# Performance work log

Measured on AMD Instinct MI355X. Metric: run time of the kernel, lower is better.

The kernel has to match this reference:

```python
import jax, jax.numpy as jnp
import numpy as np

VOCAB = 32000
DIM = 1024
BATCH = 2
SEQ = 2048
CHUNK = 256
LCTX = 4            # local_context_size, mode='sum'
LOCAL_WIN = 512     # sparse_local_window (>= 2*chunk)
GSTRIDE = 1024      # sparse_global_stride (>= 4*chunk)
LN_EPS = 1e-5


def _cache_positions():
    """Simulate the deterministic sparse KV-cache pruning per chunk (numpy, trace-time).
    Returns list of key-position index arrays (cached positions ++ current chunk)."""
    cache = np.zeros((0,), dtype=np.int64)
    per_chunk = []
    for i in range(SEQ // CHUNK):
        new = np.arange(i * CHUNK, (i + 1) * CHUNK, dtype=np.int64)
        full = np.concatenate([cache, new])
        per_chunk.append(full)
        total_seen = (i + 1) * CHUNK
        local_start = max(0, total_seen - LOCAL_WIN)
        keep = (full >= local_start) | (full % GSTRIDE == 0)
        cache = full[keep]
    return per_chunk


def setup_inputs() -> dict:
    key = jax.random.key(0)
    ks = jax.random.split(key, 8)
    s = 0.02
    return {
        "x": jax.random.randint(ks[0], (BATCH, SEQ), 0, VOCAB, dtype=jnp.int64),
        "emb_table": jax.random.normal(ks[1], (VOCAB, DIM), jnp.float32) * s,
        "q_w": jax.random.normal(ks[2], (DIM, DIM), jnp.float32) * s,
        "q_b": jnp.zeros((DIM,), jnp.float32),
        "k_w": jax.random.normal(ks[3], (DIM, DIM), jnp.float32) * s,
        "k_b": jnp.zeros((DIM,), jnp.float32),
        "v_w": jax.random.normal(ks[4], (DIM, DIM), jnp.float32) * s,
        "v_b": jnp.zeros((DIM,), jnp.float32),
        "o_w": jax.random.normal(ks[5], (DIM, DIM), jnp.float32) * s,
        "o_b": jnp.zeros((DIM,), jnp.float32),
        "ln_w": jnp.ones((DIM,), jnp.float32),
        "ln_b": jnp.zeros((DIM,), jnp.float32),
        "out_w": jax.random.normal(ks[6], (VOCAB, DIM), jnp.float32) * s,
        "out_b": jnp.zeros((VOCAB,), jnp.float32),
    }


def reference(x, emb_table, q_w, q_b, k_w, k_b, v_w, v_b, o_w, o_b, ln_w, ln_b, out_w, out_b):
    # embedding + causal local context (sum of 0..LCTX-1 shifted embeddings)
    emb = emb_table[x]                                  # [B,S,D]
    ctx = emb
    for off in range(1, LCTX):
        ctx = ctx + jnp.pad(emb, ((0, 0), (off, 0), (0, 0)))[:, :SEQ]

    # project full sequence once (same per-chunk projections in the original)
    Q = ctx @ q_w.T + q_b                               # [B,S,D]
    K = ctx @ k_w.T + k_b
    V = ctx @ v_w.T + v_b
    scale = 1.0 / np.sqrt(DIM).astype(np.float32)

    outs = []
    for i, kpos in enumerate(_cache_positions()):
        qpos = np.arange(i * CHUNK, (i + 1) * CHUNK, dtype=np.int64)
        q = Q[:, i * CHUNK:(i + 1) * CHUNK]             # [B,C,D]
        k = K[:, kpos]                                  # [B,Ki,D] gathered sparse cache + chunk
        v = V[:, kpos]
        scores = jnp.einsum('bqd,bkd->bqk', q, k) * scale
        mask = kpos[None, :] > qpos[:, None]            # [C,Ki] static causal mask
        scores = jnp.where(mask[None, :, :], -jnp.inf, scores)
        w = jax.nn.softmax(scores, axis=-1)
        outs.append(jnp.einsum('bqk,bkd->bqd', w, v))

    attended = jnp.concatenate(outs, axis=1)            # [B,S,D]
    h = attended @ o_w.T + o_b
    # LayerNorm
    mu = h.mean(-1, keepdims=True)
    var = ((h - mu) ** 2).mean(-1, keepdims=True)
    h = (h - mu) / jnp.sqrt(var + LN_EPS) * ln_w + ln_b
    return h @ out_w.T + out_b                          # [B,S,VOCAB]
```

## Files before the change

### kernel.cpp

```cpp
#include <hip/hip_runtime.h>
#include <stdint.h>

#define DIMN 1024
#define SEQN 2048
#define BATCHN 2
#define NCHUNK 8
#define CHUNKSZ 256
#define VOCABN 32000
#define ROWS_PB 6016
#define PSTRIDE_B (256*ROWS_PB)
#define LN_EPS 1e-5f

#define MBIG 4096
#define NBIG 32000
#define KBIG 1024
#define NTILES_K (KBIG/64)

typedef unsigned short ushort_t;
typedef __attribute__((ext_vector_type(8))) __bf16 bf16x8;
typedef __attribute__((ext_vector_type(4))) float f32x4;

__device__ const int d_nk[8]   = {256,512,768,769,769,769,769,770};
__device__ const int d_np[8]   = {256,512,768,896,896,896,896,896};
__device__ const int d_koff[8] = {0,256,768,1536,2432,3328,4224,5120};

__device__ __forceinline__ ushort_t f2bu(float f) {
  union { float f; unsigned u; } v; v.f = f;
  unsigned r = v.u + 0x7FFFu + ((v.u >> 16) & 1u);
  return (ushort_t)(r >> 16);
}
__device__ __forceinline__ float b2f(ushort_t u) {
  union { unsigned u; float f; } v; v.u = ((unsigned)u) << 16; return v.f;
}

__device__ __forceinline__ int pos_of(int i, int j) {
  if (i <= 2) return j;
  if (i <= 6) return (j == 0) ? 0 : (i - 3) * 256 + 255 + j;
  return (j == 0) ? 0 : ((j == 1) ? 1024 : 1278 + j);
}

__device__ __forceinline__ void gload16(const void* g, void* l) {
  __builtin_amdgcn_global_load_lds((__attribute__((address_space(1))) void*)g,
                                   (__attribute__((address_space(3))) void*)l,
                                   16, 0, 0);
}

__device__ __forceinline__ void mma_core_s(const ushort_t* __restrict__ A,
                                           const ushort_t* __restrict__ Bt,
                                           int K, ushort_t* lA, ushort_t* lB,
                                           f32x4 acc[4][4], int tid) {
  const int lane = tid & 63;
  const int wr = (tid >> 7) & 1;
  const int wc = (tid >> 6) & 1;
  const int frow = lane & 15;
  const int lhi = lane >> 4;
  const int xk = (frow & 7) << 4;
  const size_t ldb = (size_t)K * 2;
  for (int kt = 0; kt < K; kt += 64) {
#pragma unroll
    for (int t = 0; t < 4; ++t) {
      int cid = t * 256 + tid;
      int row = cid >> 3;
      int srcoff = ((cid & 7) * 16) ^ ((row & 7) << 4);
      gload16((const char*)A  + (size_t)row * ldb + (size_t)kt * 2 + srcoff,
              (char*)lA + cid * 16);
      gload16((const char*)Bt + (size_t)row * ldb + (size_t)kt * 2 + srcoff,
              (char*)lB + cid * 16);
    }
    __syncthreads();
#pragma unroll
    for (int kk = 0; kk < 2; ++kk) {
      bf16x8 af[4], bfr[4];
#pragma unroll
      for (int m = 0; m < 4; ++m) {
        int r = wr * 64 + m * 16 + frow;
        af[m] = *(const bf16x8*)((const char*)lA +
                 ((r * 128 + kk * 64 + lhi * 16) ^ xk));
      }
#pragma unroll
      for (int n = 0; n < 4; ++n) {
        int r = wc * 64 + n * 16 + frow;
        bfr[n] = *(const bf16x8*)((const char*)lB +
                  ((r * 128 + kk * 64 + lhi * 16) ^ xk));
      }
#pragma unroll
      for (int m = 0; m < 4; ++m)
#pragma unroll
        for (int n = 0; n < 4; ++n)
          acc[m][n] = __builtin_amdgcn_mfma_f32_16x16x32_bf16(af[m], bfr[n],
                                                              acc[m][n], 0, 0, 0);
    }
    __syncthreads();
  }
}

__device__ __forceinline__ void stage_tile_big(const char* Abase, const char* Bbase,
                                               ushort_t* ldsbuf, int ktile, int tid) {
  const size_t ldb = (size_t)KBIG * 2;
#pragma unroll
  for (int s = 0; s < 4; ++s) {
    const char* base = (s < 2 ? Abase : Bbase) + (size_t)(s & 1) * 128 * ldb
                       + (size_t)ktile * 128;
    ushort_t* lh = ldsbuf + s * 8192;
#pragma unroll
    for (int r2 = 0; r2 < 2; ++r2) {
      int c = r2 * 512 + tid;
      int row = c >> 3;
      int off_l = (c * 16) ^ ((row & 7) << 4);
      gload16(base + (size_t)row * ldb + (off_l & 127), (char*)lh + c * 16);
    }
  }
}

__global__ __launch_bounds__(512, 2) void k_vocab(
    const ushort_t* __restrict__ A, const ushort_t* __restrict__ Bt,
    const float* __restrict__ bias, float* __restrict__ C) {
  __shared__ ushort_t lds[2][4][8192];
  const int tid = threadIdx.x;
  const int lane = tid & 63, w = tid >> 6, wm = w >> 2, wn = w & 3;
  const int frow = lane & 15, lhi = lane >> 4;
  const int xk = (frow & 7) << 4;

  int l = blockIdx.x;
  int swz = (l & 7) * ((int)gridDim.x >> 3) + (l >> 3);
  const int mt = swz & 15;
  const int nt = swz >> 4;
  const char* Abase = (const char*)(A + (size_t)mt * 256 * KBIG);
  const char* Bbase = (const char*)(Bt + (size_t)nt * 256 * KBIG);

  f32x4 acc[8][4] = {};

  stage_tile_big(Abase, Bbase, &lds[0][0][0], 0, tid);

  for (int kt = 0; kt < NTILES_K; ++kt) {
    const int cur = kt & 1;
    __builtin_amdgcn_sched_barrier(0);
    if (kt + 1 < NTILES_K) {
      stage_tile_big(Abase, Bbase, &lds[cur ^ 1][0][0], kt + 1, tid);
      asm volatile("s_waitcnt vmcnt(8)");
    } else {
      asm volatile("s_waitcnt vmcnt(0)");
    }
    __builtin_amdgcn_s_barrier();
    __builtin_amdgcn_sched_barrier(0);

    const char* lA = (const char*)&lds[cur][wm][0];
    const char* lB = (const char*)&lds[cur][2 + (wn >> 1)][0];

    bf16x8 bF[4][2];
#pragma unroll
    for (int fc = 0; fc < 4; ++fc) {
      int c = (wn & 1) * 64 + fc * 16 + frow;
#pragma unroll
      for (int kk = 0; kk < 2; ++kk)
        bF[fc][kk] = *(const bf16x8*)(lB + ((c * 128 + kk * 64 + lhi * 16) ^ xk));
    }
#pragma unroll
    for (int q = 0; q < 4; ++q) {
      bf16x8 aF[2][2];
#pragma unroll
      for (int i = 0; i < 2; ++i) {
        int r = (2 * q + i) * 16 + frow;
#pragma unroll
        for (int kk = 0; kk < 2; ++kk)
          aF[i][kk] = *(const bf16x8*)(lA + ((r * 128 + kk * 64 + lhi * 16) ^ xk));
      }
      if (q) __builtin_amdgcn_s_barrier();
      __builtin_amdgcn_s_setprio(1);
#pragma unroll
      for (int i = 0; i < 2; ++i)
#pragma unroll
        for (int fc = 0; fc < 4; ++fc)
#pragma unroll
          for (int kk = 0; kk < 2; ++kk)
            acc[2 * q + i][fc] = __builtin_amdgcn_mfma_f32_16x16x32_bf16(
                aF[i][kk], bF[fc][kk], acc[2 * q + i][fc], 0, 0, 0);
      __builtin_amdgcn_s_setprio(0);
    }
    __builtin_amdgcn_s_barrier();
  }

  const int rbase = mt * 256 + wm * 128 + lhi * 4;
  const int cbase = nt * 256 + wn * 64 + frow;
#pragma unroll
  for (int fc = 0; fc < 4; ++fc) {
    float bv = bias[cbase + fc * 16];
#pragma unroll
    for (int fr = 0; fr < 8; ++fr)
#pragma unroll
      for (int j = 0; j < 4; ++j)
        C[(size_t)(rbase + fr * 16 + j) * NBIG + cbase + fc * 16] =
            acc[fr][fc][j] + bv;
  }
}

__global__ __launch_bounds__(256) void k_cvt(const float* __restrict__ src,
                                             ushort_t* __restrict__ dst, int n) {
  int idx = blockIdx.x * 256 + threadIdx.x;
  int stride = gridDim.x * 256;
  int n4 = n >> 2;
  for (int i = idx; i < n4; i += stride) {
    float4 v = ((const float4*)src)[i];
    ((ushort4*)dst)[i] = make_ushort4(f2bu(v.x), f2bu(v.y), f2bu(v.z), f2bu(v.w));
  }
}

__global__ __launch_bounds__(256) void k_embed(const int* __restrict__ x,
                                               const float* __restrict__ emb,
                                               ushort_t* __restrict__ ctxb) {
  const int t = blockIdx.x, b = blockIdx.y, tid = threadIdx.x;
  float4 s = make_float4(0.f, 0.f, 0.f, 0.f);
#pragma unroll
  for (int o = 0; o < 4; ++o) {
    if (t - o < 0) break;
    int tok = x[b * SEQN + t - o];
    float4 v = ((const float4*)(emb + (size_t)tok * DIMN))[tid];
    s.x += v.x; s.y += v.y; s.z += v.z; s.w += v.w;
  }
  ((ushort4*)(ctxb + ((size_t)(b * SEQN + t)) * DIMN))[tid] =
      make_ushort4(f2bu(s.x), f2bu(s.y), f2bu(s.z), f2bu(s.w));
}

__global__ __launch_bounds__(256) void k_qkv(const ushort_t* __restrict__ A,
    const ushort_t* __restrict__ Bt, const float* __restrict__ qb2,
    const float* __restrict__ kb2, const float* __restrict__ vb2,
    ushort_t* __restrict__ Qb, ushort_t* __restrict__ Kb,
    ushort_t* __restrict__ Vb) {
  __shared__ __align__(16) ushort_t lA[128*64];
  __shared__ __align__(16) ushort_t lB[128*64];
  f32x4 acc[4][4] = {};
  const int tid = threadIdx.x;
  mma_core_s(A + (size_t)blockIdx.y * 128 * KBIG,
             Bt + (size_t)blockIdx.x * 128 * KBIG, KBIG, lA, lB, acc, tid);
  const int which = blockIdx.x >> 3;
  const int col0  = (blockIdx.x & 7) * 128;
  ushort_t* Out = (which == 0) ? Qb : (which == 1) ? Kb : Vb;
  const float* Bv = (which == 0) ? qb2 : (which == 1) ? kb2 : vb2;
  const int lane = tid & 63, wr = (tid >> 7) & 1, wc = (tid >> 6) & 1;
  const int rbase = blockIdx.y * 128 + wr * 64 + (lane >> 4) * 4;
  const int cbase = col0 + wc * 64 + (lane & 15);
#pragma unroll
  for (int m = 0; m < 4; ++m)
#pragma unroll
    for (int n = 0; n < 4; ++n) {
      int c = cbase + n * 16;
      float bv = Bv[c];
#pragma unroll
      for (int j = 0; j < 4; ++j)
        Out[(size_t)(rbase + m * 16 + j) * DIMN + c] = f2bu(acc[m][n][j] + bv);
    }
}

__global__ __launch_bounds__(256) void k_gemm_f32(const ushort_t* __restrict__ A,
    const ushort_t* __restrict__ Bt, const float* __restrict__ bias,
    float* __restrict__ C, int N, int K) {
  __shared__ __align__(16) ushort_t lA[128*64];
  __shared__ __align__(16) ushort_t lB[128*64];
  f32x4 acc[4][4] = {};
  const int tid = threadIdx.x;
  mma_core_s(A + (size_t)blockIdx.y * 128 * K, Bt + (size_t)blockIdx.x * 128 * K,
             K, lA, lB, acc, tid);
  const int lane = tid & 63, wr = (tid >> 7) & 1, wc = (tid >> 6) & 1;
  const int rbase = blockIdx.y * 128 + wr * 64 + (lane >> 4) * 4;
  const int cbase = blockIdx.x * 128 + wc * 64 + (lane & 15);
#pragma unroll
  for (int m = 0; m < 4; ++m)
#pragma unroll
    for (int n = 0; n < 4; ++n) {
      int c = cbase + n * 16;
      float bv = bias[c];
#pragma unroll
      for (int j = 0; j < 4; ++j)
        C[(size_t)(rbase + m * 16 + j) * N + c] = acc[m][n][j] + bv;
    }
}

__global__ __launch_bounds__(256) void k_gatherK(const ushort_t* __restrict__ Kb,
                                                 ushort_t* __restrict__ Kg) {
  const int r = blockIdx.x, b = blockIdx.y, tid = threadIdx.x;
  int i = 7;
#pragma unroll
  for (int q = 0; q < 7; ++q) if (r < d_koff[q + 1]) { i = q; break; }
  const int j = r - d_koff[i];
  ushort4* dst = (ushort4*)(Kg + ((size_t)b * ROWS_PB + r) * DIMN);
  if (j < d_nk[i]) {
    int pos = pos_of(i, j);
    dst[tid] = ((const ushort4*)(Kb + ((size_t)b * SEQN + pos) * DIMN))[tid];
  } else {
    dst[tid] = make_ushort4(0, 0, 0, 0);
  }
}

__global__ __launch_bounds__(256) void k_transV(const ushort_t* __restrict__ Vb,
                                                ushort_t* __restrict__ VgT) {
  __shared__ ushort_t tile[64][66];
  const int z = blockIdx.z, b = z >> 3, i = z & 7;
  const int np = d_np[i], nk = d_nk[i], ko = d_koff[i];
  const int jb = blockIdx.x * 64;
  if (jb >= np) return;
  const int db = blockIdx.y * 64;
  const int tid = threadIdx.x, tx = tid & 63, ty = tid >> 6;
#pragma unroll
  for (int rep = 0; rep < 16; ++rep) {
    int jl = rep * 4 + ty;
    int j = jb + jl;
    ushort_t v = 0;
    if (j < nk) v = Vb[((size_t)b * SEQN + pos_of(i, j)) * DIMN + db + tx];
    tile[jl][tx] = v;
  }
  __syncthreads();
  const size_t base = ((size_t)b * ROWS_PB + ko) * DIMN;
#pragma unroll
  for (int rep = 0; rep < 16; ++rep) {
    int dl = rep * 4 + ty;
    VgT[base + (size_t)(db + dl) * np + jb + tx] = tile[tx][dl];
  }
}

__global__ __launch_bounds__(256) void k_scores(const ushort_t* __restrict__ Qb,
    const ushort_t* __restrict__ Kg, ushort_t* __restrict__ P) {
  const int z = blockIdx.z, b = z >> 3, i = z & 7;
  const int np = d_np[i], nk = d_nk[i], ko = d_koff[i];
  if ((int)blockIdx.x * 128 >= np) return;
  __shared__ __align__(16) ushort_t lA[128*64];
  __shared__ __align__(16) ushort_t lB[128*64];
  f32x4 acc[4][4] = {};
  const int tid = threadIdx.x;
  const ushort_t* A  = Qb + ((size_t)(b * SEQN + i * CHUNKSZ) + blockIdx.y * 128) * DIMN;
  const ushort_t* Bt = Kg + ((size_t)b * ROWS_PB + ko + blockIdx.x * 128) * DIMN;
  mma_core_s(A, Bt, DIMN, lA, lB, acc, tid);
  const int lane = tid & 63, wr = (tid >> 7) & 1, wc = (tid >> 6) & 1;
  const int rb = blockIdx.y * 128 + wr * 64 + (lane >> 4) * 4;
  const int cb = blockIdx.x * 128 + wc * 64 + (lane & 15);
  ushort_t* Pc = P + (size_t)b * PSTRIDE_B + (size_t)ko * 256;
  const float scale = 0.03125f;
  const int diag0 = nk - CHUNKSZ;
#pragma unroll
  for (int m = 0; m < 4; ++m)
#pragma unroll
    for (int n = 0; n < 4; ++n) {
      int c = cb + n * 16;
#pragma unroll
      for (int j = 0; j < 4; ++j) {
        int r = rb + m * 16 + j;
        float w = 0.0f;
        if (c < nk && (c - diag0) <= r) w = expf(acc[m][n][j] * scale);
        Pc[(size_t)r * np + c] = f2bu(w);
      }
    }
}

__global__ __launch_bounds__(256) void k_rowsum(const ushort_t* __restrict__ P,
                                                float* __restrict__ rowsum) {
  const int z = blockIdx.y, b = z >> 3, i = z & 7, r = blockIdx.x;
  const int np = d_np[i], ko = d_koff[i];
  const ushort_t* row = P + (size_t)b * PSTRIDE_B + (size_t)ko * 256 + (size_t)r * np;
  const int tid = threadIdx.x;
  float s = 0.f;
  for (int c = tid; c < np; c += 256) s += b2f(row[c]);
#pragma unroll
  for (int o = 1; o < 64; o <<= 1) s += __shfl_xor(s, o);
  __shared__ float ss[4];
  if ((tid & 63) == 0) ss[tid >> 6] = s;
  __syncthreads();
  if (tid == 0) rowsum[z * 256 + r] = ss[0] + ss[1] + ss[2] + ss[3];
}

__global__ __launch_bounds__(256) void k_pv(const ushort_t* __restrict__ P,
    const ushort_t* __restrict__ VgT, const float* __restrict__ rowsum,
    ushort_t* __restrict__ attb) {
  const int z = blockIdx.z, b = z >> 3, i = z & 7;
  const int np = d_np[i], ko = d_koff[i];
  __shared__ __align__(16) ushort_t lA[128*64];
  __shared__ __align__(16) ushort_t lB[128*64];
  f32x4 acc[4][4] = {};
  const int tid = threadIdx.x;
  const ushort_t* A  = P + (size_t)b * PSTRIDE_B + (size_t)ko * 256 +
                       (size_t)blockIdx.y * 128 * np;
  const ushort_t* Bt = VgT + ((size_t)b * ROWS_PB + ko) * DIMN +
                       (size_t)blockIdx.x * 128 * np;
  mma_core_s(A, Bt, np, lA, lB, acc, tid);
  const int lane = tid & 63, wr = (tid >> 7) & 1, wc = (tid >> 6) & 1;
  const int rb = blockIdx.y * 128 + wr * 64 + (lane >> 4) * 4;
  const int cb = blockIdx.x * 128 + wc * 64 + (lane & 15);
  const float* rs = rowsum + z * 256;
  ushort_t* outp = attb + (size_t)(b * SEQN + i * CHUNKSZ) * DIMN;
#pragma unroll
  for (int m = 0; m < 4; ++m)
#pragma unroll
    for (int j = 0; j < 4; ++j) {
      int r = rb + m * 16 + j;
      float inv = 1.0f / rs[r];
#pragma unroll
      for (int n = 0; n < 4; ++n)
        outp[(size_t)r * DIMN + cb + n * 16] = f2bu(acc[m][n][j] * inv);
    }
}

__global__ __launch_bounds__(256) void k_ln(const float* __restrict__ h,
    const float* __restrict__ lnw, const float* __restrict__ lnb,
    ushort_t* __restrict__ hb) {
  const int row = blockIdx.x, tid = threadIdx.x;
  float4 v = ((const float4*)(h + (size_t)row * DIMN))[tid];
  float s  = v.x + v.y + v.z + v.w;
  float sq = v.x * v.x + v.y * v.y + v.z * v.z + v.w * v.w;
#pragma unroll
  for (int o = 1; o < 64; o <<= 1) { s += __shfl_xor(s, o); sq += __shfl_xor(sq, o); }
  __shared__ float ss[4], ssq[4];
  if ((tid & 63) == 0) { ss[tid >> 6] = s; ssq[tid >> 6] = sq; }
  __syncthreads();
  s  = ss[0] + ss[1] + ss[2] + ss[3];
  sq = ssq[0] + ssq[1] + ssq[2] + ssq[3];
  const float mu  = s * (1.0f / DIMN);
  const float var = sq * (1.0f / DIMN) - mu * mu;
  const float inv = rsqrtf(var + LN_EPS);
  float4 w4 = ((const float4*)lnw)[tid];
  float4 b4 = ((const float4*)lnb)[tid];
  ushort4 o4 = make_ushort4(f2bu((v.x - mu) * inv * w4.x + b4.x),
                            f2bu((v.y - mu) * inv * w4.y + b4.y),
                            f2bu((v.z - mu) * inv * w4.z + b4.z),
                            f2bu((v.w - mu) * inv * w4.w + b4.w));
  ((ushort4*)(hb + (size_t)row * DIMN))[tid] = o4;
}

extern "C" void kernel_launch(void* const* d_in, const int* in_sizes, int n_in,
                              void* d_out, int out_size, void* d_ws, size_t ws_size,
                              hipStream_t stream) {
  const int*   x    = (const int*)  d_in[0];
  const float* emb  = (const float*)d_in[1];
  const float* qw   = (const float*)d_in[2];
  const float* qb   = (const float*)d_in[3];
  const float* kw   = (const float*)d_in[4];
  const float* kb   = (const float*)d_in[5];
  const float* vw   = (const float*)d_in[6];
  const float* vb   = (const float*)d_in[7];
  const float* ow   = (const float*)d_in[8];
  const float* ob   = (const float*)d_in[9];
  const float* lnw  = (const float*)d_in[10];
  const float* lnb  = (const float*)d_in[11];
  const float* outw = (const float*)d_in[12];
  const float* outb = (const float*)d_in[13];
  float* out = (float*)d_out;
  (void)in_sizes; (void)n_in; (void)out_size; (void)ws_size;

  char* ws = (char*)d_ws;
  size_t off = 0;
  auto alloc = [&](size_t bytes) {
    size_t r = off; off += (bytes + 255) & ~(size_t)255; return r;
  };
  ushort_t* wqkvb = (ushort_t*)(ws + alloc((size_t)3 * DIMN * DIMN * 2));
  ushort_t* wob   = (ushort_t*)(ws + alloc((size_t)DIMN * DIMN * 2));
  ushort_t* woutb = (ushort_t*)(ws + alloc((size_t)VOCABN * DIMN * 2));
  ushort_t* ctxb  = (ushort_t*)(ws + alloc((size_t)BATCHN * SEQN * DIMN * 2));
  ushort_t* Qb    = (ushort_t*)(ws + alloc((size_t)BATCHN * SEQN * DIMN * 2));
  ushort_t* Kb    = (ushort_t*)(ws + alloc((size_t)BATCHN * SEQN * DIMN * 2));
  ushort_t* Vb    = (ushort_t*)(ws + alloc((size_t)BATCHN * SEQN * DIMN * 2));
  ushort_t* Kg    = (ushort_t*)(ws + alloc((size_t)BATCHN * ROWS_PB * DIMN * 2));
  ushort_t* VgT   = (ushort_t*)(ws + alloc((size_t)BATCHN * ROWS_PB * DIMN * 2));
  ushort_t* Pm    = (ushort_t*)(ws + alloc((size_t)BATCHN * PSTRIDE_B * 2));
  float*    rsum  = (float*)   (ws + alloc((size_t)BATCHN * NCHUNK * 256 * 4));
  ushort_t* attb  = (ushort_t*)(ws + alloc((size_t)BATCHN * SEQN * DIMN * 2));
  float*    hbuf  = (float*)   (ws + alloc((size_t)BATCHN * SEQN * DIMN * 4));
  ushort_t* hb    = (ushort_t*)(ws + alloc((size_t)BATCHN * SEQN * DIMN * 2));

  k_cvt<<<dim3(1024), dim3(256), 0, stream>>>(qw, wqkvb,                 DIMN * DIMN);
  k_cvt<<<dim3(1024), dim3(256), 0, stream>>>(kw, wqkvb + DIMN * DIMN,   DIMN * DIMN);
  k_cvt<<<dim3(1024), dim3(256), 0, stream>>>(vw, wqkvb + 2 * DIMN * DIMN, DIMN * DIMN);
  k_cvt<<<dim3(1024), dim3(256), 0, stream>>>(ow,   wob,   DIMN * DIMN);
  k_cvt<<<dim3(2048), dim3(256), 0, stream>>>(outw, woutb, VOCABN * DIMN);

  k_embed<<<dim3(SEQN, BATCHN), dim3(256), 0, stream>>>(x, emb, ctxb);

  k_qkv<<<dim3(24, 32), dim3(256), 0, stream>>>(ctxb, wqkvb, qb, kb, vb,
                                                Qb, Kb, Vb);

  k_gatherK<<<dim3(ROWS_PB, BATCHN), dim3(256), 0, stream>>>(Kb, Kg);
  k_transV<<<dim3(14, 16, BATCHN * NCHUNK), dim3(256), 0, stream>>>(Vb, VgT);

  k_scores<<<dim3(7, 2, BATCHN * NCHUNK), dim3(256), 0, stream>>>(Qb, Kg, Pm);
  k_rowsum<<<dim3(256, BATCHN * NCHUNK), dim3(256), 0, stream>>>(Pm, rsum);
  k_pv<<<dim3(8, 2, BATCHN * NCHUNK), dim3(256), 0, stream>>>(Pm, VgT, rsum, attb);

  k_gemm_f32<<<dim3(8, 32), dim3(256), 0, stream>>>(attb, wob, ob, hbuf, DIMN, DIMN);
  k_ln<<<dim3(BATCHN * SEQN), dim3(256), 0, stream>>>(hbuf, lnw, lnb, hb);

  k_vocab<<<dim3(2000), dim3(512), 0, stream>>>(hb, woutb, outb, out);
}
```

Baseline: 604.4 us.

## Merge weight conversions, swizzle QKV grid, store o-proj output as bf16

Replaces five weight-conversion launches with one merged kernel to cut launch overhead. Remaps the QKV GEMM to a 1D grid with an XCD-style swizzle so tiles that share data land on the same chiplet and reuse cache. Writes the output projection in bf16 instead of fp32, which halves the traffic into LayerNorm at the cost of rounding h to bf16 before normalization.

```diff
diff --git a/kernel.cpp b/kernel.cpp
--- a/kernel.cpp
+++ b/kernel.cpp
@@ -194,14 +194,30 @@
   }
 }
 
-__global__ __launch_bounds__(256) void k_cvt(const float* __restrict__ src,
-                                             ushort_t* __restrict__ dst, int n) {
+#define SEG (DIMN*DIMN/4)
+__global__ __launch_bounds__(256) void k_cvt5(
+    const float* __restrict__ qw, const float* __restrict__ kw,
+    const float* __restrict__ vw, const float* __restrict__ ow,
+    const float* __restrict__ outw, ushort_t* __restrict__ wqkvb,
+    ushort_t* __restrict__ wob, ushort_t* __restrict__ woutb) {
+  const int total = 4 * SEG + (VOCABN * DIMN / 4);
   int idx = blockIdx.x * 256 + threadIdx.x;
   int stride = gridDim.x * 256;
-  int n4 = n >> 2;
-  for (int i = idx; i < n4; i += stride) {
-    float4 v = ((const float4*)src)[i];
-    ((ushort4*)dst)[i] = make_ushort4(f2bu(v.x), f2bu(v.y), f2bu(v.z), f2bu(v.w));
+  for (int i = idx; i < total; i += stride) {
+    const float4* src; ushort4* dst;
+    if (i < 3 * SEG) {
+      src = (const float4*)(i < SEG ? qw : i < 2 * SEG ? kw : vw) +
+            (i - (i < SEG ? 0 : i < 2 * SEG ? SEG : 2 * SEG));
+      dst = (ushort4*)wqkvb + i;
+    } else if (i < 4 * SEG) {
+      src = (const float4*)ow + (i - 3 * SEG);
+      dst = (ushort4*)wob + (i - 3 * SEG);
+    } else {
+      src = (const float4*)outw + (i - 4 * SEG);
+      dst = (ushort4*)woutb + (i - 4 * SEG);
+    }
+    float4 v = *src;
+    *dst = make_ushort4(f2bu(v.x), f2bu(v.y), f2bu(v.z), f2bu(v.w));
   }
 }
 
@@ -226,40 +242,44 @@
     const float* __restrict__ kb2, const float* __restrict__ vb2,
     ushort_t* __restrict__ Qb, ushort_t* __restrict__ Kb,
     ushort_t* __restrict__ Vb) {
+  int l = blockIdx.x;
+  int swz = (l & 7) * ((int)gridDim.x >> 3) + (l >> 3);
+  const int mt = swz & 31;
+  const int nt = swz >> 5;
+  __shared__ __align__(16) ushort_t lA[128*64];
+  __shared__ __align__(16) ushort_t lB[128*64];
+  f32x4 acc[4][4] = {};
+  const int tid = threadIdx.x;
+  mma_core_s(A + (size_t)mt * 128 * KBIG,
+             Bt + (size_t)nt * 128 * KBIG, KBIG, lA, lB, acc, tid);
+  const int which = nt >> 3;
+  const int col0  = (nt & 7) * 128;
+  ushort_t* Out = (which == 0) ? Qb : (which == 1) ? Kb : Vb;
+  const float* Bv = (which == 0) ? qb2 : (which == 1) ? kb2 : vb2;
+  const int lane = tid & 63, wr = (tid >> 7) & 1, wc = (tid >> 6) & 1;
+  const int rbase = mt * 128 + wr * 64 + (lane >> 4) * 4;
+  const int cbase = col0 + wc * 64 + (lane & 15);
+#pragma unroll
+  for (int m = 0; m < 4; ++m)
+#pragma unroll
+    for (int n = 0; n < 4; ++n) {
+      int c = cbase + n * 16;
+      float bv = Bv[c];
+#pragma unroll
+      for (int j = 0; j < 4; ++j)
+        Out[(size_t)(rbase + m * 16 + j) * DIMN + c] = f2bu(acc[m][n][j] + bv);
+    }
+}
+
+__global__ __launch_bounds__(256) void k_oproj(const ushort_t* __restrict__ A,
+    const ushort_t* __restrict__ Bt, const float* __restrict__ bias,
+    ushort_t* __restrict__ C) {
   __shared__ __align__(16) ushort_t lA[128*64];
   __shared__ __align__(16) ushort_t lB[128*64];
   f32x4 acc[4][4] = {};
   const int tid = threadIdx.x;
   mma_core_s(A + (size_t)blockIdx.y * 128 * KBIG,
              Bt + (size_t)blockIdx.x * 128 * KBIG, KBIG, lA, lB, acc, tid);
-  const int which = blockIdx.x >> 3;
-  const int col0  = (blockIdx.x & 7) * 128;
-  ushort_t* Out = (which == 0) ? Qb : (which == 1) ? Kb : Vb;
-  const float* Bv = (which == 0) ? qb2 : (which == 1) ? kb2 : vb2;
-  const int lane = tid & 63, wr = (tid >> 7) & 1, wc = (tid >> 6) & 1;
-  const int rbase = blockIdx.y * 128 + wr * 64 + (lane >> 4) * 4;
-  const int cbase = col0 + wc * 64 + (lane & 15);
-#pragma unroll
-  for (int m = 0; m < 4; ++m)
-#pragma unroll
-    for (int n = 0; n < 4; ++n) {
-      int c = cbase + n * 16;
-      float bv = Bv[c];
-#pragma unroll
-      for (int j = 0; j < 4; ++j)
-        Out[(size_t)(rbase + m * 16 + j) * DIMN + c] = f2bu(acc[m][n][j] + bv);
-    }
-}
-
-__global__ __launch_bounds__(256) void k_gemm_f32(const ushort_t* __restrict__ A,
-    const ushort_t* __restrict__ Bt, const float* __restrict__ bias,
-    float* __restrict__ C, int N, int K) {
-  __shared__ __align__(16) ushort_t lA[128*64];
-  __shared__ __align__(16) ushort_t lB[128*64];
-  f32x4 acc[4][4] = {};
-  const int tid = threadIdx.x;
-  mma_core_s(A + (size_t)blockIdx.y * 128 * K, Bt + (size_t)blockIdx.x * 128 * K,
-             K, lA, lB, acc, tid);
   const int lane = tid & 63, wr = (tid >> 7) & 1, wc = (tid >> 6) & 1;
   const int rbase = blockIdx.y * 128 + wr * 64 + (lane >> 4) * 4;
   const int cbase = blockIdx.x * 128 + wc * 64 + (lane & 15);
@@ -271,7 +291,7 @@
       float bv = bias[c];
 #pragma unroll
       for (int j = 0; j < 4; ++j)
-        C[(size_t)(rbase + m * 16 + j) * N + c] = acc[m][n][j] + bv;
+        C[(size_t)(rbase + m * 16 + j) * DIMN + c] = f2bu(acc[m][n][j] + bv);
     }
 }
 
@@ -397,11 +417,12 @@
     }
 }
 
-__global__ __launch_bounds__(256) void k_ln(const float* __restrict__ h,
+__global__ __launch_bounds__(256) void k_ln(const ushort_t* __restrict__ h,
     const float* __restrict__ lnw, const float* __restrict__ lnb,
     ushort_t* __restrict__ hb) {
   const int row = blockIdx.x, tid = threadIdx.x;
-  float4 v = ((const float4*)(h + (size_t)row * DIMN))[tid];
+  ushort4 u4 = ((const ushort4*)(h + (size_t)row * DIMN))[tid];
+  float4 v = make_float4(b2f(u4.x), b2f(u4.y), b2f(u4.z), b2f(u4.w));
   float s  = v.x + v.y + v.z + v.w;
   float sq = v.x * v.x + v.y * v.y + v.z * v.z + v.w * v.w;
 #pragma unroll
@@ -460,19 +481,16 @@
   ushort_t* Pm    = (ushort_t*)(ws + alloc((size_t)BATCHN * PSTRIDE_B * 2));
   float*    rsum  = (float*)   (ws + alloc((size_t)BATCHN * NCHUNK * 256 * 4));
   ushort_t* attb  = (ushort_t*)(ws + alloc((size_t)BATCHN * SEQN * DIMN * 2));
-  float*    hbuf  = (float*)   (ws + alloc((size_t)BATCHN * SEQN * DIMN * 4));
+  ushort_t* hbuf  = (ushort_t*)(ws + alloc((size_t)BATCHN * SEQN * DIMN * 2));
   ushort_t* hb    = (ushort_t*)(ws + alloc((size_t)BATCHN * SEQN * DIMN * 2));
 
-  k_cvt<<<dim3(1024), dim3(256), 0, stream>>>(qw, wqkvb,                 DIMN * DIMN);
-  k_cvt<<<dim3(1024), dim3(256), 0, stream>>>(kw, wqkvb + DIMN * DIMN,   DIMN * DIMN);
-  k_cvt<<<dim3(1024), dim3(256), 0, stream>>>(vw, wqkvb + 2 * DIMN * DIMN, DIMN * DIMN);
-  k_cvt<<<dim3(1024), dim3(256), 0, stream>>>(ow,   wob,   DIMN * DIMN);
-  k_cvt<<<dim3(2048), dim3(256), 0, stream>>>(outw, woutb, VOCABN * DIMN);
+  k_cvt5<<<dim3(4096), dim3(256), 0, stream>>>(qw, kw, vw, ow, outw,
+                                               wqkvb, wob, woutb);
 
   k_embed<<<dim3(SEQN, BATCHN), dim3(256), 0, stream>>>(x, emb, ctxb);
 
-  k_qkv<<<dim3(24, 32), dim3(256), 0, stream>>>(ctxb, wqkvb, qb, kb, vb,
-                                                Qb, Kb, Vb);
+  k_qkv<<<dim3(768), dim3(256), 0, stream>>>(ctxb, wqkvb, qb, kb, vb,
+                                             Qb, Kb, Vb);
 
   k_gatherK<<<dim3(ROWS_PB, BATCHN), dim3(256), 0, stream>>>(Kb, Kg);
   k_transV<<<dim3(14, 16, BATCHN * NCHUNK), dim3(256), 0, stream>>>(Vb, VgT);
@@ -481,7 +499,7 @@
   k_rowsum<<<dim3(256, BATCHN * NCHUNK), dim3(256), 0, stream>>>(Pm, rsum);
   k_pv<<<dim3(8, 2, BATCHN * NCHUNK), dim3(256), 0, stream>>>(Pm, VgT, rsum, attb);
 
-  k_gemm_f32<<<dim3(8, 32), dim3(256), 0, stream>>>(attb, wob, ob, hbuf, DIMN, DIMN);
+  k_oproj<<<dim3(8, 32), dim3(256), 0, stream>>>(attb, wob, ob, hbuf);
   k_ln<<<dim3(BATCHN * SEQN), dim3(256), 0, stream>>>(hbuf, lnw, lnb, hb);
 
   k_vocab<<<dim3(2000), dim3(512), 0, stream>>>(hb, woutb, outb, out);
```

Measured after the change: 589.2 us. -2.5%, faster.
